# Kernel optimization log

Measured on AMD Instinct MI355X. Metric: run time of the kernel, lower is better.

## Reference

```python
import jax, jax.numpy as jnp
import numpy as np

N_NODES = 100000
N_FEAT = 512
HIDDEN = 64
N_CLASSES = 40
N_EDGES = 3200000
K = 10
ALPHA = 0.1


def setup_inputs() -> dict:
    key = jax.random.key(0)
    k1, k2, k3, k4 = jax.random.split(key, 4)
    x = jax.random.normal(k1, (N_NODES, N_FEAT), dtype=jnp.float32)
    # Glorot-ish scaled linear weights
    W1 = jax.random.normal(k2, (N_FEAT, HIDDEN), dtype=jnp.float32) / np.sqrt(N_FEAT)
    b1 = jnp.zeros((HIDDEN,), dtype=jnp.float32)
    W2 = jax.random.normal(k3, (HIDDEN, N_CLASSES), dtype=jnp.float32) / np.sqrt(HIDDEN)
    b2 = jnp.zeros((N_CLASSES,), dtype=jnp.float32)
    edge_index = jax.random.randint(k4, (2, N_EDGES), 0, N_NODES, dtype=jnp.int64)
    return {"x": x, "W1": W1, "b1": b1, "W2": W2, "b2": b2, "edge_index": edge_index}


def reference(x, W1, b1, W2, b2, edge_index):
    n = x.shape[0]
    # MLP (dropout is identity in eval mode)
    h = jnp.maximum(x @ W1 + b1, 0.0)
    h = h @ W2 + b2  # [N, C]

    # gcn_norm with self-loops: A_hat = D^{-1/2} (A + I) D^{-1/2}
    loops = jnp.arange(n, dtype=edge_index.dtype)
    row = jnp.concatenate([edge_index[0], loops])  # source (gather)
    col = jnp.concatenate([edge_index[1], loops])  # target (scatter)
    deg = jax.ops.segment_sum(jnp.ones(row.shape, dtype=h.dtype), col, num_segments=n)
    dinv = jnp.where(deg > 0, jax.lax.rsqrt(deg), 0.0)
    norm = dinv[row] * dinv[col]  # [E + N]

    h0 = h

    def step(z, _):
        msg = norm[:, None] * z[row]                      # gather + scale
        agg = jax.ops.segment_sum(msg, col, num_segments=n)  # scatter-add
        z = ALPHA * h0 + (1.0 - ALPHA) * agg
        return z, None

    z, _ = jax.lax.scan(step, h0, None, length=K)
    return jax.nn.log_softmax(z, axis=1)
```

## Files before the change

### kernel.cpp

```cpp
#include <hip/hip_runtime.h>
#include <hip/hip_bf16.h>
#include <hip/hip_fp16.h>

#define N_NODES   100000
#define N_FEAT    512
#define HIDDEN    64
#define N_CLASSES 40
#define KITER     10
#define ALPHA     0.1f
#define HPITCH    72
#define NXCD      8
#define WIN       (N_NODES / NXCD)
#define NPH       4
#define SRCWIN    (N_NODES / NPH)
#define SUBCAP    131072
#define PARTB     2048
#define CAP       128
#define N40       ((size_t)N_NODES * 40)

typedef __attribute__((ext_vector_type(8))) short bf16x8;
typedef __attribute__((ext_vector_type(4))) float f32x4;

__device__ __forceinline__ float bf2f(unsigned short u) {
    union { unsigned int i; float f; } c;
    c.i = ((unsigned int)u) << 16;
    return c.f;
}
__device__ __forceinline__ unsigned short f2bf(float f) {
    union { float f; unsigned int u; } c; c.f = f;
    unsigned int r = c.u + 0x7FFFu + ((c.u >> 16) & 1u);
    return (unsigned short)(r >> 16);
}

__global__ void zero_cur_kernel(int* __restrict__ cur, int* __restrict__ flags) {
    int t = threadIdx.x;
    if (t < 33) cur[t] = 0;
    if (t >= 33 && t < 35) flags[t - 33] = 0;
}

__global__ void detect_float_kernel(const unsigned short* __restrict__ w1raw,
                                    int* __restrict__ flags) {
    int i = blockIdx.x * blockDim.x + threadIdx.x;
    if (i < 32768) {
        unsigned short u = w1raw[i];
        if ((u & 0x7F80u) == 0x7F80u) atomicAdd(&flags[0], 1);
    }
}

__global__ void detect_edge_kernel(const int* __restrict__ ei, int* __restrict__ flags) {
    int i = blockIdx.x * blockDim.x + threadIdx.x;
    if (i < 2048) {
        if (ei[2 * i + 1] != 0) atomicAdd(&flags[1], 1);
    }
}

__global__ void pack_w1_kernel(const void* __restrict__ W1p, const int* __restrict__ flags,
                               unsigned short* __restrict__ pb) {
    int idx = blockIdx.x * 256 + threadIdx.x;
    int j    = idx & 7;
    int lane = (idx >> 3) & 63;
    int ktnt = idx >> 9;
    int kt = ktnt & 15, nt = ktnt >> 4;
    int k = kt * 32 + (lane >> 4) * 8 + j;
    int n = nt * 16 + (lane & 15);
    unsigned short v;
    if (flags[0] > 0) v = f2bf(((const float*)W1p)[k * HIDDEN + n]);
    else              v = ((const unsigned short*)W1p)[k * HIDDEN + n];
    pb[idx] = v;
}

__global__ void pack_w2_kernel(const void* __restrict__ W2p, const int* __restrict__ flags,
                               unsigned short* __restrict__ pb2) {
    int idx = blockIdx.x * 256 + threadIdx.x;
    if (idx >= 3072) return;
    int j    = idx & 7;
    int lane = (idx >> 3) & 63;
    int ktnt = idx >> 9;
    int kt = ktnt & 1, nt = ktnt >> 1;
    int k = kt * 32 + (lane >> 4) * 8 + j;
    int n = nt * 16 + (lane & 15);
    unsigned short v = 0;
    if (n < N_CLASSES) {
        if (flags[0] > 0) v = f2bf(((const float*)W2p)[k * N_CLASSES + n]);
        else              v = ((const unsigned short*)W2p)[k * N_CLASSES + n];
    }
    pb2[idx] = v;
}

__global__ __launch_bounds__(256) void mlp_kernel(
    const void* __restrict__ xp,
    const unsigned short* __restrict__ pb,
    const unsigned short* __restrict__ pb2,
    const void* __restrict__ b1p,
    const void* __restrict__ b2p,
    const int* __restrict__ flags,
    const float* __restrict__ dinv,
    float* __restrict__ h0,
    __half* __restrict__ y0)
{
    __shared__ unsigned short hsb[4][16 * HPITCH];
    const int t    = threadIdx.x;
    const int wave = t >> 6;
    const int lane = t & 63;
    const int quad = lane >> 4;
    const int ml   = lane & 15;
    const int mbase = blockIdx.x * 64 + wave * 16;
    const int isf32 = flags[0] > 0;
    const bool valid = mbase < N_NODES;

    const bf16x8* pbv = (const bf16x8*)pb;
    f32x4 acc[4];
    #pragma unroll
    for (int nt = 0; nt < 4; ++nt) acc[nt] = (f32x4){0.f, 0.f, 0.f, 0.f};

    if (valid) {
        if (!isf32) {
            const unsigned short* xrow = (const unsigned short*)xp
                                       + (size_t)(mbase + ml) * N_FEAT + quad * 8;
            #pragma unroll
            for (int kt = 0; kt < 16; ++kt) {
                bf16x8 a = *(const bf16x8*)(xrow + kt * 32);
                #pragma unroll
                for (int nt = 0; nt < 4; ++nt)
                    acc[nt] = __builtin_amdgcn_mfma_f32_16x16x32_bf16(
                        a, pbv[(nt * 16 + kt) * 64 + lane], acc[nt], 0, 0, 0);
            }
        } else {
            const float* xf = (const float*)xp + (size_t)(mbase + ml) * N_FEAT + quad * 8;
            #pragma unroll
            for (int kt = 0; kt < 16; ++kt) {
                float4 lo = *(const float4*)(xf + kt * 32);
                float4 hi = *(const float4*)(xf + kt * 32 + 4);
                bf16x8 a;
                a[0] = (short)f2bf(lo.x); a[1] = (short)f2bf(lo.y);
                a[2] = (short)f2bf(lo.z); a[3] = (short)f2bf(lo.w);
                a[4] = (short)f2bf(hi.x); a[5] = (short)f2bf(hi.y);
                a[6] = (short)f2bf(hi.z); a[7] = (short)f2bf(hi.w);
                #pragma unroll
                for (int nt = 0; nt < 4; ++nt)
                    acc[nt] = __builtin_amdgcn_mfma_f32_16x16x32_bf16(
                        a, pbv[(nt * 16 + kt) * 64 + lane], acc[nt], 0, 0, 0);
            }
        }

        #pragma unroll
        for (int nt = 0; nt < 4; ++nt) {
            float b1v = isf32 ? ((const float*)b1p)[nt * 16 + ml]
                              : bf2f(((const unsigned short*)b1p)[nt * 16 + ml]);
            #pragma unroll
            for (int r = 0; r < 4; ++r)
                hsb[wave][(quad * 4 + r) * HPITCH + nt * 16 + ml] =
                    f2bf(fmaxf(acc[nt][r] + b1v, 0.0f));
        }
    }
    __syncthreads();

    if (valid) {
        const bf16x8* pb2v = (const bf16x8*)pb2;
        f32x4 acc2[3];
        #pragma unroll
        for (int n2 = 0; n2 < 3; ++n2) acc2[n2] = (f32x4){0.f, 0.f, 0.f, 0.f};
        #pragma unroll
        for (int kt = 0; kt < 2; ++kt) {
            bf16x8 a = *(const bf16x8*)(&hsb[wave][ml * HPITCH + kt * 32 + quad * 8]);
            #pragma unroll
            for (int n2 = 0; n2 < 3; ++n2)
                acc2[n2] = __builtin_amdgcn_mfma_f32_16x16x32_bf16(
                    a, pb2v[(n2 * 2 + kt) * 64 + lane], acc2[n2], 0, 0, 0);
        }
        #pragma unroll
        for (int n2 = 0; n2 < 3; ++n2) {
            int n = n2 * 16 + ml;
            if (n < N_CLASSES) {
                float b2v = isf32 ? ((const float*)b2p)[n]
                                  : bf2f(((const unsigned short*)b2p)[n]);
                #pragma unroll
                for (int r = 0; r < 4; ++r) {
                    int node = mbase + quad * 4 + r;
                    float v = acc2[n2][r] + b2v;
                    h0[(size_t)node * N_CLASSES + n] = v;
                    y0[(size_t)node * 40 + n] = __float2half(v * dinv[node]);
                }
            }
        }
    }
}

__global__ void zero_pad_kernel(__half* __restrict__ a, __half* __restrict__ b) {
    int t = threadIdx.x;
    __half z = __float2half(0.0f);
    if (t < 48)             a[N40 + t] = z;
    else if (t < 96)        b[N40 + (t - 48)] = z;
}

__global__ __launch_bounds__(256) void partition_kernel(
    const int* __restrict__ ei, const int* __restrict__ flags,
    unsigned int* __restrict__ sub,
    int* __restrict__ cur, int2* __restrict__ ovf, int E)
{
    __shared__ unsigned buf[32][CAP];
    __shared__ int cnt_lds[32];
    __shared__ unsigned base_s[32];

    const int i64f = flags[1] == 0;
    const int per  = (E + PARTB - 1) / PARTB;
    const int e0   = blockIdx.x * per;
    const int e1   = min(e0 + per, E);

    if (threadIdx.x < 32) cnt_lds[threadIdx.x] = 0;
    __syncthreads();

    for (int e = e0 + threadIdx.x; e < e1; e += 256) {
        int c = i64f ? __builtin_nontemporal_load(ei + 2 * E + 2 * e)
                     : __builtin_nontemporal_load(ei + E + e);
        int r = i64f ? __builtin_nontemporal_load(ei + 2 * e)
                     : __builtin_nontemporal_load(ei + e);
        int wd = c / WIN;
        int sp = r / SRCWIN;
        int b  = wd * 4 + sp;
        unsigned pk = (unsigned)r | ((unsigned)(c - wd * WIN) << 17);
        int slot = atomicAdd(&cnt_lds[b], 1);
        if (slot < CAP) buf[b][slot] = pk;
        else { int op = atomicAdd(cur + 32, 1); ovf[op] = make_int2(r, c); }
    }
    __syncthreads();

    const int g  = threadIdx.x >> 3;
    const int l8 = threadIdx.x & 7;
    const int n  = min(cnt_lds[g], CAP);
    if (l8 == 0 && n > 0) base_s[g] = (unsigned)atomicAdd(&cur[g], n);
    __syncthreads();
    if (n > 0) {
        unsigned base = base_s[g];
        unsigned bslot = (unsigned)g * SUBCAP;
        for (int i = l8; i < n; i += 8) {
            unsigned p = base + (unsigned)i;
            unsigned pk = buf[g][i];
            if (p < SUBCAP) sub[bslot + p] = pk;
            else {
                int op = atomicAdd(cur + 32, 1);
                ovf[op] = make_int2((int)(pk & 0x1FFFFu),
                                    (g >> 2) * WIN + (int)(pk >> 17));
            }
        }
    }
}

__global__ __launch_bounds__(1024) void hist_kernel(
    const unsigned int* __restrict__ sub, const int* __restrict__ cur,
    const int2* __restrict__ ovf, int* __restrict__ hists)
{
    __shared__ int h[WIN];
    const int w = blockIdx.x & 7;
    const int s = blockIdx.x >> 3;
    const int b = w * 4 + s;
    for (int off = threadIdx.x; off < WIN; off += 1024) h[off] = 0;
    __syncthreads();
    int n = min(cur[b], SUBCAP);
    const unsigned int* sp = sub + (size_t)b * SUBCAP;
    for (int i = threadIdx.x; i < n; i += 1024)
        atomicAdd(&h[sp[i] >> 17], 1);
    if (s == 3) {
        int ov = cur[32];
        for (int i = threadIdx.x; i < ov; i += 1024) {
            int2 rc = ovf[i];
            int ww = rc.y / WIN;
            if (ww == w) atomicAdd(&h[rc.y - ww * WIN], 1);
        }
    }
    __syncthreads();
    for (int off = threadIdx.x; off < WIN; off += 1024)
        hists[(size_t)b * WIN + off] = h[off];
}

__global__ void cnt_kernel(const int* __restrict__ hists, int* __restrict__ cnt,
                           float* __restrict__ dinv) {
    int i = blockIdx.x * 256 + threadIdx.x;
    if (i >= N_NODES) return;
    int w = i / WIN, off = i - w * WIN;
    int c = 0;
    #pragma unroll
    for (int x = 0; x < 4; ++x) c += hists[(size_t)(w * 4 + x) * WIN + off];
    cnt[i] = c;
    dinv[i] = rsqrtf((float)c + 1.0f);
}

__global__ __launch_bounds__(1024) void scan_kernel(
    const int* __restrict__ cnt, int* __restrict__ rptr, int E)
{
    __shared__ int wsum[16];
    __shared__ int carry_s, tiletot_s;
    const int t = threadIdx.x, wave = t >> 6, lane = t & 63;
    if (t == 0) carry_s = 0;
    __syncthreads();
    for (int base = 0; base < N_NODES; base += 4096) {
        int i0 = base + t * 4;
        int v0 = (i0 + 0 < N_NODES) ? cnt[i0 + 0] : 0;
        int v1 = (i0 + 1 < N_NODES) ? cnt[i0 + 1] : 0;
        int v2 = (i0 + 2 < N_NODES) ? cnt[i0 + 2] : 0;
        int v3 = (i0 + 3 < N_NODES) ? cnt[i0 + 3] : 0;
        int tl = v0 + v1 + v2 + v3;
        int sc = tl;
        #pragma unroll
        for (int off = 1; off < 64; off <<= 1) {
            int u = __shfl_up(sc, off, 64);
            if (lane >= off) sc += u;
        }
        if (lane == 63) wsum[wave] = sc;
        int wexcl = sc - tl;
        __syncthreads();
        if (wave == 0) {
            int wv = (lane < 16) ? wsum[lane] : 0;
            int ws = wv;
            #pragma unroll
            for (int off = 1; off < 16; off <<= 1) {
                int u = __shfl_up(ws, off, 64);
                if (lane >= off) ws += u;
            }
            if (lane < 16) wsum[lane] = ws - wv;
            if (lane == 15) tiletot_s = ws;
        }
        __syncthreads();
        int P  = carry_s + wsum[wave] + wexcl;
        if (i0 + 0 < N_NODES) rptr[i0 + 0] = P;
        if (i0 + 1 < N_NODES) rptr[i0 + 1] = P + v0;
        if (i0 + 2 < N_NODES) rptr[i0 + 2] = P + v0 + v1;
        if (i0 + 3 < N_NODES) rptr[i0 + 3] = P + v0 + v1 + v2;
        __syncthreads();
        if (t == 0) carry_s += tiletot_s;
        __syncthreads();
    }
    if (t == 0) rptr[N_NODES] = E;
}

__global__ __launch_bounds__(1024) void scatter_kernel(
    const unsigned int* __restrict__ sub, const int* __restrict__ cur,
    const int* __restrict__ hists, const int2* __restrict__ ovf,
    const int* __restrict__ rptr, int* __restrict__ srcidx, int* __restrict__ soff)
{
    __shared__ int curs[WIN];
    const int w = blockIdx.x & 7;
    const int s = blockIdx.x >> 3;
    const int b = w * 4 + s;
    for (int off = threadIdx.x; off < WIN; off += 1024) {
        int node = w * WIN + off;
        int base = rptr[node];
        for (int x = 0; x < s; ++x)
            base += hists[(size_t)(w * 4 + x) * WIN + off];
        curs[off] = base;
        soff[node * 4 + s] = base;
    }
    __syncthreads();
    int n = min(cur[b], SUBCAP);
    const unsigned int* sp = sub + (size_t)b * SUBCAP;
    for (int i = threadIdx.x; i < n; i += 1024) {
        unsigned pk = sp[i];
        int slot = atomicAdd(&curs[pk >> 17], 1);
        srcidx[slot] = (int)(pk & 0x1FFFFu);
    }
    if (s == 3) {
        int ov = cur[32];
        for (int i = threadIdx.x; i < ov; i += 1024) {
            int2 rc = ovf[i];
            int ww = rc.y / WIN;
            if (ww == w) {
                int slot = atomicAdd(&curs[rc.y - ww * WIN], 1);
                srcidx[slot] = rc.x;
            }
        }
    }
}

__global__ __launch_bounds__(256) void phase_kernel(
    const __half* __restrict__ yin, const int* __restrict__ soff,
    const int* __restrict__ rptr, const int* __restrict__ srcidx,
    float* __restrict__ partial)
{
    const int p    = blockIdx.x & 3;
    const int nb   = blockIdx.x >> 2;
    const int wave = threadIdx.x >> 6;
    const int lane = threadIdx.x & 63;
    const int g    = lane >> 4;
    const int l    = lane & 15;
    const int node = nb * 16 + wave * 4 + g;
    const int c0   = l * 4;
    const int offr = (l < 10) ? l * 4 : 0;

    const int start = soff[node * 4 + p];
    const int end   = (p < 3) ? soff[node * 4 + p + 1] : rptr[node + 1];
    int nch = (end - start + 15) >> 4;
    int m1    = max(nch, __shfl_xor(nch, 16, 64));
    int maxch = max(m1,  __shfl_xor(m1, 32, 64));

    float a0 = 0.f, a1 = 0.f, a2 = 0.f, a3 = 0.f;
    float b0 = 0.f, b1 = 0.f, b2 = 0.f, b3 = 0.f;

    for (int ch = 0; ch < maxch; ++ch) {
        int idx = start + ch * 16 + l;
        int sw  = (idx < end) ? srcidx[idx] : N_NODES;

        #pragma unroll
        for (int i = 0; i < 16; i += 2) {
            int s0 = __shfl(sw, (g << 4) + i,     64);
            int s1 = __shfl(sw, (g << 4) + i + 1, 64);
            uint2 z0 = *(const uint2*)(yin + (size_t)s0 * 40 + offr);
            uint2 z1 = *(const uint2*)(yin + (size_t)s1 * 40 + offr);
            const __half2* p0 = (const __half2*)&z0;
            const __half2* p1 = (const __half2*)&z1;
            float2 f00 = __half22float2(p0[0]);
            float2 f01 = __half22float2(p0[1]);
            float2 f10 = __half22float2(p1[0]);
            float2 f11 = __half22float2(p1[1]);
            a0 += f00.x; a1 += f00.y; a2 += f01.x; a3 += f01.y;
            b0 += f10.x; b1 += f10.y; b2 += f11.x; b3 += f11.y;
        }
    }

    if (c0 < N_CLASSES) {
        f32x4 o;
        o[0] = a0 + b0; o[1] = a1 + b1; o[2] = a2 + b2; o[3] = a3 + b3;
        f32x4* dst = (f32x4*)(partial + (size_t)p * N40 + (size_t)node * 40 + c0);
        __builtin_nontemporal_store(o, dst);
    }
}

__global__ __launch_bounds__(256) void reduce_kernel(
    const float* __restrict__ partial, const __half* __restrict__ yin,
    const float* __restrict__ h0, const float* __restrict__ dinv,
    __half* __restrict__ yout)
{
    const int wave = threadIdx.x >> 6;
    const int lane = threadIdx.x & 63;
    const int g    = lane >> 4;
    const int l    = lane & 15;
    const int node = blockIdx.x * 16 + wave * 4 + g;
    const int c0   = l * 4;
    if (c0 >= N_CLASSES) return;

    float sx = 0.f, sy = 0.f, sz = 0.f, sw = 0.f;
    #pragma unroll
    for (int p = 0; p < NPH; ++p) {
        f32x4 v = *(const f32x4*)(partial + (size_t)p * N40 + (size_t)node * 40 + c0);
        sx += v[0]; sy += v[1]; sz += v[2]; sw += v[3];
    }
    uint2 ys = *(const uint2*)(yin + (size_t)node * 40 + c0);
    f32x4 h = *(const f32x4*)(h0 + (size_t)node * 40 + c0);
    float di = dinv[node];
    const __half2* ps = (const __half2*)&ys;
    float2 s01 = __half22float2(ps[0]);
    float2 s23 = __half22float2(ps[1]);
    float kk = (1.0f - ALPHA) * di;
    float o0 = ALPHA * h[0] + kk * (sx + s01.x);
    float o1 = ALPHA * h[1] + kk * (sy + s01.y);
    float o2 = ALPHA * h[2] + kk * (sz + s23.x);
    float o3 = ALPHA * h[3] + kk * (sw + s23.y);
    __half2 q01 = __floats2half2_rn(di * o0, di * o1);
    __half2 q23 = __floats2half2_rn(di * o2, di * o3);
    uint2 st;
    st.x = *(unsigned int*)&q01;
    st.y = *(unsigned int*)&q23;
    *(uint2*)(yout + (size_t)node * 40 + c0) = st;
}

__global__ __launch_bounds__(256) void lsm_kernel(
    const __half* __restrict__ y, const float* __restrict__ dinv,
    const int* __restrict__ flags, void* __restrict__ outp)
{
    const int wave = threadIdx.x >> 6;
    const int lane = threadIdx.x & 63;
    const int node = blockIdx.x * 4 + wave;
    const int isf32 = flags[0] > 0;

    float di = dinv[node];
    float v = (lane < N_CLASSES)
            ? __half2float(y[(size_t)node * 40 + lane]) / di : -1e30f;
    float m = v;
    #pragma unroll
    for (int o = 32; o; o >>= 1) m = fmaxf(m, __shfl_xor(m, o, 64));
    float e = (lane < N_CLASSES) ? expf(v - m) : 0.0f;
    float s = e;
    #pragma unroll
    for (int o = 32; o; o >>= 1) s += __shfl_xor(s, o, 64);
    float ls = logf(s);
    if (lane < N_CLASSES) {
        float r = v - m - ls;
        size_t idx = (size_t)node * N_CLASSES + lane;
        if (isf32) ((float*)outp)[idx] = r;
        else       ((__hip_bfloat16*)outp)[idx] = __float2bfloat16(r);
    }
}

extern "C" void kernel_launch(void* const* d_in, const int* in_sizes, int n_in,
                              void* d_out, int out_size, void* d_ws, size_t ws_size,
                              hipStream_t stream)
{
    const void* x  = d_in[0];
    const void* W1 = d_in[1];
    const void* b1 = d_in[2];
    const void* W2 = d_in[3];
    const void* b2 = d_in[4];
    const int* ei = (const int*)d_in[5];
    const int E = in_sizes[5] / 2;

    char* ws = (char*)d_ws;
    size_t off = 0;
    auto carve = [&](size_t bytes) -> void* {
        void* p = ws + off;
        off = (off + bytes + 255) & ~(size_t)255;
        return p;
    };
    float*  h0    = (float*) carve((size_t)N_NODES * N_CLASSES * 4);
    __half* yA    = (__half*)carve((N40 + 64) * 2);
    __half* yB    = (__half*)carve((N40 + 64) * 2);
    float*  partial = (float*)carve((size_t)NPH * N40 * 4);
    int*    cnt   = (int*)   carve((size_t)N_NODES * 4);
    float*  dinv  = (float*) carve((size_t)N_NODES * 4);
    int*    rptr  = (int*)   carve((size_t)(N_NODES + 1) * 4);
    int*    soff  = (int*)   carve((size_t)N_NODES * 4 * 4);
    int*    srcidx= (int*)   carve((size_t)E * 4);
    unsigned int* sub = (unsigned int*)carve((size_t)32 * SUBCAP * 4);
    int*    hists = (int*)   carve((size_t)32 * WIN * 4);
    int2*   ovf   = (int2*)  carve((size_t)E * 8);
    int*    cur   = (int*)   carve(33 * sizeof(int));
    unsigned short* pb  = (unsigned short*)carve(32768 * 2);
    unsigned short* pb2 = (unsigned short*)carve(3072 * 2);
    int*    flags = (int*)   carve(2 * sizeof(int));
    (void)ws_size; (void)n_in; (void)out_size;

    const int nodeBlocks  = N_NODES / 4;
    const int mlpBlocks   = (N_NODES + 63) / 64;
    const int nodeBlocks16= N_NODES / 16;
    const int phaseBlocks = nodeBlocks16 * NPH;
    const int cntBlocks   = (N_NODES + 255) / 256;

    zero_cur_kernel<<<1, 64, 0, stream>>>(cur, flags);
    detect_float_kernel<<<128, 256, 0, stream>>>((const unsigned short*)W1, flags);
    detect_edge_kernel<<<8, 256, 0, stream>>>(ei, flags);
    pack_w1_kernel<<<128, 256, 0, stream>>>(W1, flags, pb);
    pack_w2_kernel<<<12, 256, 0, stream>>>(W2, flags, pb2);

    partition_kernel<<<PARTB, 256, 0, stream>>>(ei, flags, sub, cur, ovf, E);
    hist_kernel<<<32, 1024, 0, stream>>>(sub, cur, ovf, hists);
    cnt_kernel<<<cntBlocks, 256, 0, stream>>>(hists, cnt, dinv);
    scan_kernel<<<1, 1024, 0, stream>>>(cnt, rptr, E);
    scatter_kernel<<<32, 1024, 0, stream>>>(sub, cur, hists, ovf, rptr, srcidx, soff);
    zero_pad_kernel<<<1, 128, 0, stream>>>(yA, yB);

    mlp_kernel<<<mlpBlocks, 256, 0, stream>>>(x, pb, pb2, b1, b2, flags, dinv, h0, yA);

    const __half* yin = yA;
    __half* yout = yB;
    const __half* ylast = yA;
    for (int it = 0; it < KITER; ++it) {
        phase_kernel<<<phaseBlocks, 256, 0, stream>>>(yin, soff, rptr, srcidx, partial);
        reduce_kernel<<<nodeBlocks16, 256, 0, stream>>>(partial, yin, h0, dinv, yout);
        ylast = yout;
        yin = yout;
        yout = (yout == yB) ? yA : yB;
    }

    lsm_kernel<<<nodeBlocks, 256, 0, stream>>>(ylast, dinv, flags, d_out);
}
```

Measured before the change: 1.277 ms.

## Fuse phase, reduce and log-softmax into one propagation kernel with padded rows

Drops the four-way source-window phase split and its fp32 partial-sum buffer. One prop_kernel now gathers each node's whole CSR neighbour list, applies the alpha/h0 update in registers, and on the last iteration computes log_softmax and writes the output directly. The fp16 feature rows are padded from 40 to 64 halves so gathers use aligned shift-based addressing, and the next chunk of srcidx is prefetched. This removes the partial-buffer writes and reads plus two launches per iteration, but gives up the L2 locality the source-window split provided and enlarges the gathered working set.

```diff
diff --git a/kernel.cpp b/kernel.cpp
--- a/kernel.cpp
+++ b/kernel.cpp
@@ -11,12 +11,11 @@
 #define HPITCH    72
 #define NXCD      8
 #define WIN       (N_NODES / NXCD)
-#define NPH       4
-#define SRCWIN    (N_NODES / NPH)
+#define NSB       4
+#define SRCWIN    (N_NODES / NSB)
 #define SUBCAP    131072
 #define PARTB     2048
 #define CAP       128
-#define N40       ((size_t)N_NODES * 40)
 
 typedef __attribute__((ext_vector_type(8))) short bf16x8;
 typedef __attribute__((ext_vector_type(4))) float f32x4;
@@ -179,7 +178,7 @@
                     int node = mbase + quad * 4 + r;
                     float v = acc2[n2][r] + b2v;
                     h0[(size_t)node * N_CLASSES + n] = v;
-                    y0[(size_t)node * 40 + n] = __float2half(v * dinv[node]);
+                    y0[((size_t)node << 6) + n] = __float2half(v * dinv[node]);
                 }
             }
         }
@@ -189,8 +188,8 @@
 __global__ void zero_pad_kernel(__half* __restrict__ a, __half* __restrict__ b) {
     int t = threadIdx.x;
     __half z = __float2half(0.0f);
-    if (t < 48)             a[N40 + t] = z;
-    else if (t < 96)        b[N40 + (t - 48)] = z;
+    if (t < 64)             a[((size_t)N_NODES << 6) + t] = z;
+    else if (t < 128)       b[((size_t)N_NODES << 6) + (t - 64)] = z;
 }
 
 __global__ __launch_bounds__(256) void partition_kernel(
@@ -336,7 +335,7 @@
 __global__ __launch_bounds__(1024) void scatter_kernel(
     const unsigned int* __restrict__ sub, const int* __restrict__ cur,
     const int* __restrict__ hists, const int2* __restrict__ ovf,
-    const int* __restrict__ rptr, int* __restrict__ srcidx, int* __restrict__ soff)
+    const int* __restrict__ rptr, int* __restrict__ srcidx)
 {
     __shared__ int curs[WIN];
     const int w = blockIdx.x & 7;
@@ -348,7 +347,6 @@
         for (int x = 0; x < s; ++x)
             base += hists[(size_t)(w * 4 + x) * WIN + off];
         curs[off] = base;
-        soff[node * 4 + s] = base;
     }
     __syncthreads();
     int n = min(cur[b], SUBCAP);
@@ -371,40 +369,49 @@
     }
 }
 
-__global__ __launch_bounds__(256) void phase_kernel(
-    const __half* __restrict__ yin, const int* __restrict__ soff,
-    const int* __restrict__ rptr, const int* __restrict__ srcidx,
-    float* __restrict__ partial)
-{
-    const int p    = blockIdx.x & 3;
-    const int nb   = blockIdx.x >> 2;
+__global__ __launch_bounds__(256) void prop_kernel(
+    const __half* __restrict__ zh, const float* __restrict__ h0,
+    const float* __restrict__ dinv, const int* __restrict__ rptr,
+    const int* __restrict__ srcidx, __half* __restrict__ zout,
+    const int* __restrict__ flags, void* __restrict__ outp, int last)
+{
     const int wave = threadIdx.x >> 6;
     const int lane = threadIdx.x & 63;
     const int g    = lane >> 4;
     const int l    = lane & 15;
-    const int node = nb * 16 + wave * 4 + g;
+    const int node = blockIdx.x * 16 + wave * 4 + g;
     const int c0   = l * 4;
-    const int offr = (l < 10) ? l * 4 : 0;
-
-    const int start = soff[node * 4 + p];
-    const int end   = (p < 3) ? soff[node * 4 + p + 1] : rptr[node + 1];
-    int nch = (end - start + 15) >> 4;
+
+    const int beg = rptr[node];
+    const int end = rptr[node + 1];
+    int nch = (end - beg + 15) >> 4;
     int m1    = max(nch, __shfl_xor(nch, 16, 64));
     int maxch = max(m1,  __shfl_xor(m1, 32, 64));
 
+    float di = dinv[node];
+    uint2 yself = *(const uint2*)(zh + ((size_t)node << 6) + c0);
+    float h00 = 0.f, h01 = 0.f, h02 = 0.f, h03 = 0.f;
+    if (c0 < N_CLASSES) {
+        const float* hp = h0 + (size_t)node * N_CLASSES + c0;
+        h00 = hp[0]; h01 = hp[1]; h02 = hp[2]; h03 = hp[3];
+    }
+
     float a0 = 0.f, a1 = 0.f, a2 = 0.f, a3 = 0.f;
     float b0 = 0.f, b1 = 0.f, b2 = 0.f, b3 = 0.f;
 
+    int idx0 = beg + l;
+    int sw = (idx0 < end) ? srcidx[idx0] : N_NODES;
+
     for (int ch = 0; ch < maxch; ++ch) {
-        int idx = start + ch * 16 + l;
-        int sw  = (idx < end) ? srcidx[idx] : N_NODES;
+        int idxn = beg + (ch + 1) * 16 + l;
+        int swn = (ch + 1 < maxch) ? ((idxn < end) ? srcidx[idxn] : N_NODES) : N_NODES;
 
         #pragma unroll
         for (int i = 0; i < 16; i += 2) {
             int s0 = __shfl(sw, (g << 4) + i,     64);
             int s1 = __shfl(sw, (g << 4) + i + 1, 64);
-            uint2 z0 = *(const uint2*)(yin + (size_t)s0 * 40 + offr);
-            uint2 z1 = *(const uint2*)(yin + (size_t)s1 * 40 + offr);
+            uint2 z0 = *(const uint2*)(zh + ((size_t)s0 << 6) + c0);
+            uint2 z1 = *(const uint2*)(zh + ((size_t)s1 << 6) + c0);
             const __half2* p0 = (const __half2*)&z0;
             const __half2* p1 = (const __half2*)&z1;
             float2 f00 = __half22float2(p0[0]);
@@ -414,79 +421,57 @@
             a0 += f00.x; a1 += f00.y; a2 += f01.x; a3 += f01.y;
             b0 += f10.x; b1 += f10.y; b2 += f11.x; b3 += f11.y;
         }
-    }
-
+        sw = swn;
+    }
+
+    float o0 = 0.f, o1 = 0.f, o2 = 0.f, o3 = 0.f;
     if (c0 < N_CLASSES) {
-        f32x4 o;
-        o[0] = a0 + b0; o[1] = a1 + b1; o[2] = a2 + b2; o[3] = a3 + b3;
-        f32x4* dst = (f32x4*)(partial + (size_t)p * N40 + (size_t)node * 40 + c0);
-        __builtin_nontemporal_store(o, dst);
-    }
-}
-
-__global__ __launch_bounds__(256) void reduce_kernel(
-    const float* __restrict__ partial, const __half* __restrict__ yin,
-    const float* __restrict__ h0, const float* __restrict__ dinv,
-    __half* __restrict__ yout)
-{
-    const int wave = threadIdx.x >> 6;
-    const int lane = threadIdx.x & 63;
-    const int g    = lane >> 4;
-    const int l    = lane & 15;
-    const int node = blockIdx.x * 16 + wave * 4 + g;
-    const int c0   = l * 4;
-    if (c0 >= N_CLASSES) return;
-
-    float sx = 0.f, sy = 0.f, sz = 0.f, sw = 0.f;
-    #pragma unroll
-    for (int p = 0; p < NPH; ++p) {
-        f32x4 v = *(const f32x4*)(partial + (size_t)p * N40 + (size_t)node * 40 + c0);
-        sx += v[0]; sy += v[1]; sz += v[2]; sw += v[3];
-    }
-    uint2 ys = *(const uint2*)(yin + (size_t)node * 40 + c0);
-    f32x4 h = *(const f32x4*)(h0 + (size_t)node * 40 + c0);
-    float di = dinv[node];
-    const __half2* ps = (const __half2*)&ys;
-    float2 s01 = __half22float2(ps[0]);
-    float2 s23 = __half22float2(ps[1]);
-    float kk = (1.0f - ALPHA) * di;
-    float o0 = ALPHA * h[0] + kk * (sx + s01.x);
-    float o1 = ALPHA * h[1] + kk * (sy + s01.y);
-    float o2 = ALPHA * h[2] + kk * (sz + s23.x);
-    float o3 = ALPHA * h[3] + kk * (sw + s23.y);
-    __half2 q01 = __floats2half2_rn(di * o0, di * o1);
-    __half2 q23 = __floats2half2_rn(di * o2, di * o3);
-    uint2 st;
-    st.x = *(unsigned int*)&q01;
-    st.y = *(unsigned int*)&q23;
-    *(uint2*)(yout + (size_t)node * 40 + c0) = st;
-}
-
-__global__ __launch_bounds__(256) void lsm_kernel(
-    const __half* __restrict__ y, const float* __restrict__ dinv,
-    const int* __restrict__ flags, void* __restrict__ outp)
-{
-    const int wave = threadIdx.x >> 6;
-    const int lane = threadIdx.x & 63;
-    const int node = blockIdx.x * 4 + wave;
-    const int isf32 = flags[0] > 0;
-
-    float di = dinv[node];
-    float v = (lane < N_CLASSES)
-            ? __half2float(y[(size_t)node * 40 + lane]) / di : -1e30f;
-    float m = v;
-    #pragma unroll
-    for (int o = 32; o; o >>= 1) m = fmaxf(m, __shfl_xor(m, o, 64));
-    float e = (lane < N_CLASSES) ? expf(v - m) : 0.0f;
-    float s = e;
-    #pragma unroll
-    for (int o = 32; o; o >>= 1) s += __shfl_xor(s, o, 64);
-    float ls = logf(s);
-    if (lane < N_CLASSES) {
-        float r = v - m - ls;
-        size_t idx = (size_t)node * N_CLASSES + lane;
-        if (isf32) ((float*)outp)[idx] = r;
-        else       ((__hip_bfloat16*)outp)[idx] = __float2bfloat16(r);
+        const __half2* ps = (const __half2*)&yself;
+        float2 s01 = __half22float2(ps[0]);
+        float2 s23 = __half22float2(ps[1]);
+        float kk = (1.0f - ALPHA) * di;
+        o0 = ALPHA * h00 + kk * (a0 + b0 + s01.x);
+        o1 = ALPHA * h01 + kk * (a1 + b1 + s01.y);
+        o2 = ALPHA * h02 + kk * (a2 + b2 + s23.x);
+        o3 = ALPHA * h03 + kk * (a3 + b3 + s23.y);
+    }
+
+    if (!last) {
+        if (c0 < N_CLASSES) {
+            __half2 q01 = __floats2half2_rn(di * o0, di * o1);
+            __half2 q23 = __floats2half2_rn(di * o2, di * o3);
+            uint2 st;
+            st.x = *(unsigned int*)&q01;
+            st.y = *(unsigned int*)&q23;
+            *(uint2*)(zout + ((size_t)node << 6) + c0) = st;
+        }
+    } else {
+        float mx = (c0 < N_CLASSES) ? fmaxf(fmaxf(o0, o1), fmaxf(o2, o3)) : -1e30f;
+        #pragma unroll
+        for (int msk = 1; msk < 16; msk <<= 1)
+            mx = fmaxf(mx, __shfl_xor(mx, msk, 16));
+        float es = (c0 < N_CLASSES)
+                 ? (expf(o0 - mx) + expf(o1 - mx) + expf(o2 - mx) + expf(o3 - mx))
+                 : 0.0f;
+        #pragma unroll
+        for (int msk = 1; msk < 16; msk <<= 1)
+            es += __shfl_xor(es, msk, 16);
+        float ls = logf(es);
+        if (c0 < N_CLASSES) {
+            size_t idx = (size_t)node * N_CLASSES + c0;
+            float r0 = o0 - mx - ls, r1 = o1 - mx - ls;
+            float r2 = o2 - mx - ls, r3 = o3 - mx - ls;
+            if (flags[0] > 0) {
+                float* op = (float*)outp;
+                op[idx] = r0; op[idx + 1] = r1; op[idx + 2] = r2; op[idx + 3] = r3;
+            } else {
+                __hip_bfloat16* op = (__hip_bfloat16*)outp;
+                op[idx]     = __float2bfloat16(r0);
+                op[idx + 1] = __float2bfloat16(r1);
+                op[idx + 2] = __float2bfloat16(r2);
+                op[idx + 3] = __float2bfloat16(r3);
+            }
+        }
     }
 }
 
@@ -510,13 +495,11 @@
         return p;
     };
     float*  h0    = (float*) carve((size_t)N_NODES * N_CLASSES * 4);
-    __half* yA    = (__half*)carve((N40 + 64) * 2);
-    __half* yB    = (__half*)carve((N40 + 64) * 2);
-    float*  partial = (float*)carve((size_t)NPH * N40 * 4);
+    __half* yA    = (__half*)carve(((size_t)(N_NODES + 1) << 6) * 2);
+    __half* yB    = (__half*)carve(((size_t)(N_NODES + 1) << 6) * 2);
     int*    cnt   = (int*)   carve((size_t)N_NODES * 4);
     float*  dinv  = (float*) carve((size_t)N_NODES * 4);
     int*    rptr  = (int*)   carve((size_t)(N_NODES + 1) * 4);
-    int*    soff  = (int*)   carve((size_t)N_NODES * 4 * 4);
     int*    srcidx= (int*)   carve((size_t)E * 4);
     unsigned int* sub = (unsigned int*)carve((size_t)32 * SUBCAP * 4);
     int*    hists = (int*)   carve((size_t)32 * WIN * 4);
@@ -527,10 +510,8 @@
     int*    flags = (int*)   carve(2 * sizeof(int));
     (void)ws_size; (void)n_in; (void)out_size;
 
-    const int nodeBlocks  = N_NODES / 4;
     const int mlpBlocks   = (N_NODES + 63) / 64;
-    const int nodeBlocks16= N_NODES / 16;
-    const int phaseBlocks = nodeBlocks16 * NPH;
+    const int propBlocks  = N_NODES / 16;
     const int cntBlocks   = (N_NODES + 255) / 256;
 
     zero_cur_kernel<<<1, 64, 0, stream>>>(cur, flags);
@@ -543,21 +524,18 @@
     hist_kernel<<<32, 1024, 0, stream>>>(sub, cur, ovf, hists);
     cnt_kernel<<<cntBlocks, 256, 0, stream>>>(hists, cnt, dinv);
     scan_kernel<<<1, 1024, 0, stream>>>(cnt, rptr, E);
-    scatter_kernel<<<32, 1024, 0, stream>>>(sub, cur, hists, ovf, rptr, srcidx, soff);
+    scatter_kernel<<<32, 1024, 0, stream>>>(sub, cur, hists, ovf, rptr, srcidx);
     zero_pad_kernel<<<1, 128, 0, stream>>>(yA, yB);
 
     mlp_kernel<<<mlpBlocks, 256, 0, stream>>>(x, pb, pb2, b1, b2, flags, dinv, h0, yA);
 
     const __half* yin = yA;
     __half* yout = yB;
-    const __half* ylast = yA;
     for (int it = 0; it < KITER; ++it) {
-        phase_kernel<<<phaseBlocks, 256, 0, stream>>>(yin, soff, rptr, srcidx, partial);
-        reduce_kernel<<<nodeBlocks16, 256, 0, stream>>>(partial, yin, h0, dinv, yout);
-        ylast = yout;
+        int last = (it == KITER - 1) ? 1 : 0;
+        prop_kernel<<<propBlocks, 256, 0, stream>>>(yin, h0, dinv, rptr, srcidx,
+                                                    yout, flags, d_out, last);
         yin = yout;
         yout = (yout == yB) ? yA : yB;
     }
-
-    lsm_kernel<<<nodeBlocks, 256, 0, stream>>>(ylast, dinv, flags, d_out);
-}
+}
```

Result: faster. 1.049 ms (-17.9%).
